# Kernel tuning notes

Measured on AMD Instinct MI355X. Metric: run time of the kernel, lower is better.

Reference implementation:

```python
import jax, jax.numpy as jnp
import numpy as np

N = 8192
E_DIM = 256
HID = 256
OUT = 128
N_PRED = 2_000_000


def setup_inputs() -> dict:
    key = jax.random.key(0)
    ks = jax.random.split(key, 6)
    node_indices = jnp.arange(N, dtype=jnp.int64) if jax.config.jax_enable_x64 else jnp.arange(N, dtype=jnp.int32)
    attn_matrix = jax.random.normal(ks[0], (N, N), dtype=jnp.float32)
    edge_label_index = jax.random.randint(ks[1], (2, N_PRED), 0, N)
    emb = jax.random.normal(ks[2], (N, E_DIM), dtype=jnp.float32) * 0.05
    W1 = jax.random.normal(ks[3], (E_DIM, HID), dtype=jnp.float32) * (1.0 / np.sqrt(E_DIM))
    b1 = jnp.zeros((HID,), dtype=jnp.float32)
    W2 = jax.random.normal(ks[4], (HID, OUT), dtype=jnp.float32) * (1.0 / np.sqrt(HID))
    b2 = jnp.zeros((OUT,), dtype=jnp.float32)
    return {"node_indices": node_indices, "attn_matrix": attn_matrix,
            "edge_label_index": edge_label_index, "emb": emb,
            "W1": W1, "b1": b1, "W2": W2, "b2": b2}


def reference(node_indices, attn_matrix, edge_label_index, emb, W1, b1, W2, b2):
    # dense_to_sparse of an (almost surely) all-nonzero dense matrix keeps all
    # N^2 edges (incl. diagonal), so no extra self-loops are added by gcn_norm.
    w = jax.nn.relu(attn_matrix)                       # edge weights after F.relu
    deg = w.sum(axis=0)                                # deg[j] = sum_i w[i,j] (scatter on col)
    dis = jnp.where(deg > 0, jax.lax.rsqrt(deg), 0.0)  # deg^{-1/2}, inf -> 0
    a_norm = dis[:, None] * w * dis[None, :]           # norm_ij = d_i^-1/2 w_ij d_j^-1/2

    x = emb[node_indices]                              # embedding lookup [N, E_DIM]
    # GCNConv: aggregate transformed features at target (col): out = A_norm^T @ (x W) + b
    h = jax.nn.relu(a_norm.T @ (x @ W1) + b1)          # [N, HID]
    z = a_norm.T @ (h @ W2) + b2                       # [N, OUT]

    # decode: dot product between endpoint embeddings
    scores = jnp.einsum('ed,ed->e', z[edge_label_index[0]], z[edge_label_index[1]])
    return scores
```

## Files before the change

### kernel.cpp

```cpp
#include <hip/hip_runtime.h>

typedef _Float16 half8  __attribute__((ext_vector_type(8)));
typedef _Float16 half4v __attribute__((ext_vector_type(4)));
typedef _Float16 half2v __attribute__((ext_vector_type(2)));
typedef float    floatx4 __attribute__((ext_vector_type(4)));
typedef float    f4v     __attribute__((ext_vector_type(4)));

#define NND 8192
#define PA  40
#define PT  136

__device__ __forceinline__ int swzk(int m, int k) { return k ^ (((m >> 3) & 3) << 3); }

#define GLOAD16(gp, lp) __builtin_amdgcn_global_load_lds(                        \
    (const __attribute__((address_space(1))) void*)(gp),                         \
    (__attribute__((address_space(3))) void*)(lp), 16, 0, 0)

#define VMCNT0() asm volatile("s_waitcnt vmcnt(0)" ::: "memory")

__global__ __launch_bounds__(256) void k_degT(const float* __restrict__ A,
                                              _Float16* __restrict__ Wh,
                                              float* __restrict__ deg) {
    __shared__ _Float16 T[128 * PT];
    __shared__ float sdeg[8 * 128];
    int t  = threadIdx.x;
    int j0 = blockIdx.x * 128, i0 = blockIdx.y * 128;
    int c = t & 31;
    int g = t >> 5;

    f4v s = {0.f, 0.f, 0.f, 0.f};
    #pragma unroll
    for (int p = 0; p < 2; ++p) {
        int rb = 64 * p + 8 * g;
        f4v v[8];
        #pragma unroll
        for (int rr = 0; rr < 8; ++rr)
            v[rr] = *(const f4v*)(A + (size_t)(i0 + rb + rr) * NND + j0 + 4 * c);
        #pragma unroll
        for (int rr = 0; rr < 8; ++rr)
            #pragma unroll
            for (int u = 0; u < 4; ++u) v[rr][u] = fmaxf(v[rr][u], 0.f);
        #pragma unroll
        for (int u = 0; u < 4; ++u) {
            half8 hv;
            #pragma unroll
            for (int rr = 0; rr < 8; ++rr) { hv[rr] = (_Float16)v[rr][u]; s[u] += v[rr][u]; }
            *(half8*)(&T[(4 * c + u) * PT + rb]) = hv;
        }
    }
    *(f4v*)(&sdeg[g * 128 + 4 * c]) = s;
    __syncthreads();

    if (t < 128) {
        float d = 0.f;
        #pragma unroll
        for (int g2 = 0; g2 < 8; ++g2) d += sdeg[g2 * 128 + t];
        atomicAdd(&deg[j0 + t], d);
    }

    #pragma unroll
    for (int p = 0; p < 8; ++p) {
        int j  = 16 * p + (t >> 4);
        int ic = (t & 15) * 8;
        half8 hv = *(const half8*)(&T[j * PT + ic]);
        *(half8*)(Wh + (size_t)(j0 + j) * NND + i0 + ic) = hv;
    }
}

__global__ __launch_bounds__(256) void k_dis(const float* __restrict__ deg, float* __restrict__ dis) {
    int j = blockIdx.x * 256 + threadIdx.x;
    float d = deg[j];
    dis[j] = d > 0.f ? 1.f / sqrtf(d) : 0.f;
}

template <typename AT>
__global__ __launch_bounds__(256) void k_mm_small(
    const AT* __restrict__ Abase, const int* __restrict__ gather,
    const float* __restrict__ B, int NB,
    _Float16* __restrict__ outT, const float* __restrict__ dis, float out_scale) {

    __shared__ _Float16 As[128 * PA];
    __shared__ _Float16 Bs[64 * PA];

    int t  = threadIdx.x;
    int i0 = blockIdx.x * 128;
    int n0 = blockIdx.y * 64;

    int am = t & 127, akh = t >> 7;
    int row = i0 + am;
    if (gather) row = gather[row];
    const AT* arow = Abase + (size_t)row * 256;

    int tp = t & 15, kp = t >> 4;

    int lane = t & 63, w = t >> 6;
    int wm = w & 1, wn = w >> 1;
    int lm = lane & 15, q = lane >> 4;

    floatx4 acc[4][2];
    #pragma unroll
    for (int a = 0; a < 4; ++a)
        #pragma unroll
        for (int b = 0; b < 2; ++b) acc[a][b] = (floatx4){0.f, 0.f, 0.f, 0.f};

    for (int ks = 0; ks < 8; ++ks) {
        int c0 = ks * 32;

        half8 av[2];
        if constexpr (sizeof(AT) == 4) {
            #pragma unroll
            for (int cc = 0; cc < 2; ++cc) {
                f4v v0 = *(const f4v*)(arow + c0 + akh * 16 + cc * 8);
                f4v v1 = *(const f4v*)(arow + c0 + akh * 16 + cc * 8 + 4);
                half8 hv;
                #pragma unroll
                for (int e = 0; e < 4; ++e) {
                    hv[e]     = (_Float16)(16.f * v0[e]);
                    hv[4 + e] = (_Float16)(16.f * v1[e]);
                }
                av[cc] = hv;
            }
        } else {
            av[0] = *(const half8*)(arow + c0 + akh * 16);
            av[1] = *(const half8*)(arow + c0 + akh * 16 + 8);
        }

        const float* bp = B + (size_t)(c0 + 2 * kp) * NB + n0 + 4 * tp;
        f4v r0 = *(const f4v*)bp;
        f4v r1 = *(const f4v*)(bp + NB);

        __syncthreads();
        #pragma unroll
        for (int cc = 0; cc < 2; ++cc) {
            int k = akh * 16 + cc * 8;
            *(half8*)(&As[am * PA + swzk(am, k)]) = av[cc];
        }
        #pragma unroll
        for (int u = 0; u < 4; ++u) {
            int n = 4 * tp + u;
            half2v p = {(_Float16)r0[u], (_Float16)r1[u]};
            *(half2v*)(&Bs[n * PA + swzk(n, 2 * kp)]) = p;
        }
        __syncthreads();

        half8 af[4], bf[2];
        #pragma unroll
        for (int mt = 0; mt < 4; ++mt) {
            int m = wm * 64 + mt * 16 + lm;
            af[mt] = *(const half8*)(&As[m * PA + swzk(m, q * 8)]);
        }
        #pragma unroll
        for (int nt = 0; nt < 2; ++nt) {
            int n = wn * 32 + nt * 16 + lm;
            bf[nt] = *(const half8*)(&Bs[n * PA + swzk(n, q * 8)]);
        }
        #pragma unroll
        for (int mt = 0; mt < 4; ++mt)
            #pragma unroll
            for (int nt = 0; nt < 2; ++nt)
                acc[mt][nt] = __builtin_amdgcn_mfma_f32_16x16x32_f16(af[mt], bf[nt], acc[mt][nt], 0, 0, 0);
    }

    #pragma unroll
    for (int mt = 0; mt < 4; ++mt) {
        int ib = i0 + wm * 64 + mt * 16 + q * 4;
        #pragma unroll
        for (int nt = 0; nt < 2; ++nt) {
            int n = n0 + wn * 32 + nt * 16 + lm;
            #pragma unroll
            for (int r = 0; r < 4; ++r) {
                float v = acc[mt][nt][r] * dis[ib + r] * out_scale;
                outT[(size_t)n * NND + ib + r] = (_Float16)v;
            }
        }
    }
}

template <int BN>
__global__ __launch_bounds__(256) void k_mm_big(
    const _Float16* __restrict__ Wh, const _Float16* __restrict__ Bt, float* __restrict__ Cp) {

    __shared__ __align__(16) _Float16 As[2 * 128 * 32];
    __shared__ __align__(16) _Float16 Bs[2 * 128 * 32];

    int t = threadIdx.x;
    int j0 = blockIdx.x * 128;
    int n0 = blockIdx.y * 128;
    size_t i_begin = (size_t)blockIdx.z * 1024;
    float* C = Cp + (size_t)blockIdx.z * (size_t)NND * BN;

    int lane = t & 63, w = t >> 6;
    int wm = w & 1, wn = w >> 1;
    int lm = lane & 15, q = lane >> 4;

    int srow = lane >> 2;
    int scol = (lane & 3) * 8;
    const _Float16* aS0 = Wh + (size_t)(j0 + w * 16 + srow) * NND + i_begin + scol;
    const _Float16* aS1 = aS0 + (size_t)64 * NND;
    const _Float16* bS0 = Bt + (size_t)(n0 + w * 16 + srow) * NND + i_begin + scol;
    const _Float16* bS1 = bS0 + (size_t)64 * NND;

    char* aLb = (char*)As + w * 1024;
    char* bLb = (char*)Bs + w * 1024;

    floatx4 acc[4][4];
    #pragma unroll
    for (int a = 0; a < 4; ++a)
        #pragma unroll
        for (int b = 0; b < 4; ++b) acc[a][b] = (floatx4){0.f, 0.f, 0.f, 0.f};

    {
        GLOAD16(aS0, aLb);
        GLOAD16(aS1, aLb + 4096);
        GLOAD16(bS0, bLb);
        GLOAD16(bS1, bLb + 4096);
    }
    VMCNT0();
    __builtin_amdgcn_s_barrier();

    for (int ks = 0; ks < 32; ++ks) {
        int cur = ks & 1;
        const _Float16* Ab = As + cur * 4096;
        const _Float16* Bb = Bs + cur * 4096;

        if (ks < 31) {
            int ko = (ks + 1) * 32;
            char* aL = aLb + (cur ^ 1) * 8192;
            char* bL = bLb + (cur ^ 1) * 8192;
            GLOAD16(aS0 + ko, aL);
            GLOAD16(aS1 + ko, aL + 4096);
            GLOAD16(bS0 + ko, bL);
            GLOAD16(bS1 + ko, bL + 4096);
        }

        half8 af[4], bf[4];
        #pragma unroll
        for (int mt = 0; mt < 4; ++mt) {
            int m = wm * 64 + mt * 16 + lm;
            af[mt] = *(const half8*)(&Ab[m * 32 + q * 8]);
        }
        #pragma unroll
        for (int nt = 0; nt < 4; ++nt) {
            int n = wn * 64 + nt * 16 + lm;
            bf[nt] = *(const half8*)(&Bb[n * 32 + q * 8]);
        }
        #pragma unroll
        for (int mt = 0; mt < 4; ++mt)
            #pragma unroll
            for (int nt = 0; nt < 4; ++nt)
                acc[mt][nt] = __builtin_amdgcn_mfma_f32_16x16x32_f16(af[mt], bf[nt], acc[mt][nt], 0, 0, 0);

        VMCNT0();
        __builtin_amdgcn_s_barrier();
    }

    #pragma unroll
    for (int mt = 0; mt < 4; ++mt) {
        int rb = j0 + wm * 64 + mt * 16 + q * 4;
        #pragma unroll
        for (int nt = 0; nt < 4; ++nt) {
            int col = n0 + wn * 64 + nt * 16 + lm;
            #pragma unroll
            for (int r = 0; r < 4; ++r)
                C[(size_t)(rb + r) * BN + col] = acc[mt][nt][r];
        }
    }
}

template <int NSH, bool RELU>
__global__ __launch_bounds__(256) void k_finalize(const float* __restrict__ Cp, const float* __restrict__ dis,
                                                  const float* __restrict__ bias, _Float16* __restrict__ out) {
    int idx4 = (blockIdx.x * 256 + threadIdx.x) * 4;
    f4v v = {0.f, 0.f, 0.f, 0.f};
    #pragma unroll
    for (int z = 0; z < 8; ++z) {
        f4v p = *(const f4v*)(Cp + (size_t)z * (NND << NSH) + idx4);
        #pragma unroll
        for (int r = 0; r < 4; ++r) v[r] += p[r];
    }
    int j  = idx4 >> NSH;
    int n0 = idx4 & ((1 << NSH) - 1);
    float dj = dis[j] * (1.f / 1024.f);
    f4v b4 = *(const f4v*)(bias + n0);
    half4v o;
    #pragma unroll
    for (int r = 0; r < 4; ++r) {
        float x = v[r] * dj + b4[r];
        if (RELU) x = fmaxf(x, 0.f);
        o[r] = (_Float16)(x * 64.f);
    }
    *(half4v*)(out + idx4) = o;
}

__global__ __launch_bounds__(256) void k_edges(const _Float16* __restrict__ zh, const int* __restrict__ ei,
                                               float* __restrict__ out, int npred) {
    int g = (blockIdx.x * 256 + threadIdx.x) >> 4;
    int l = threadIdx.x & 15;
    if (g >= npred) return;
    int a = ei[g], b = ei[npred + g];
    half8 za = *(const half8*)(zh + (size_t)a * 128 + l * 8);
    half8 zb = *(const half8*)(zh + (size_t)b * 128 + l * 8);
    float s = 0.f;
    #pragma unroll
    for (int e = 0; e < 4; ++e) {
        half2v a2 = {za[2 * e], za[2 * e + 1]};
        half2v b2 = {zb[2 * e], zb[2 * e + 1]};
        s = __builtin_amdgcn_fdot2(a2, b2, s, false);
    }
    s += __shfl_xor(s, 1);
    s += __shfl_xor(s, 2);
    s += __shfl_xor(s, 4);
    s += __shfl_xor(s, 8);
    if (l == 0) out[g] = s * (1.f / 4096.f);
}

extern "C" void kernel_launch(void* const* d_in, const int* in_sizes, int n_in,
                              void* d_out, int out_size, void* d_ws, size_t ws_size,
                              hipStream_t stream) {
    const int*   nodes = (const int*)d_in[0];
    const float* attn  = (const float*)d_in[1];
    const int*   eidx  = (const int*)d_in[2];
    const float* emb   = (const float*)d_in[3];
    const float* W1    = (const float*)d_in[4];
    const float* b1    = (const float*)d_in[5];
    const float* W2    = (const float*)d_in[6];
    const float* b2    = (const float*)d_in[7];
    float* out = (float*)d_out;
    int npred = in_sizes[2] / 2;

    char* ws = (char*)d_ws;
    float*    deg = (float*)(ws);
    float*    dis = (float*)(ws + 0x8000);
    _Float16* Wh  = (_Float16*)(ws + 0x10000);
    float*    C1p = (float*)(ws + 0x8010000);
    float*    C2p = (float*)(ws + 0xC010000);
    _Float16* M1p = (_Float16*)(ws + 0xE010000);
    _Float16* h   = (_Float16*)(ws + 0xE410000);
    _Float16* M2p = (_Float16*)(ws + 0xE810000);
    _Float16* zh  = (_Float16*)(ws + 0xEA10000);

    hipMemsetAsync(deg, 0, 8192 * sizeof(float), stream);

    k_degT<<<dim3(64, 64), 256, 0, stream>>>(attn, Wh, deg);
    k_dis<<<32, 256, 0, stream>>>(deg, dis);

    k_mm_small<float><<<dim3(64, 4), 256, 0, stream>>>(emb, nodes, W1, 256, M1p, dis, 64.f);
    k_mm_big<256><<<dim3(64, 2, 8), 256, 0, stream>>>(Wh, M1p, C1p);
    k_finalize<8, true><<<2048, 256, 0, stream>>>(C1p, dis, b1, h);
    k_mm_small<_Float16><<<dim3(64, 2), 256, 0, stream>>>(h, nullptr, W2, 128, M2p, dis, 16.f);
    k_mm_big<128><<<dim3(64, 1, 8), 256, 0, stream>>>(Wh, M2p, C2p);
    k_finalize<7, false><<<1024, 256, 0, stream>>>(C2p, dis, b2, zh);

    k_edges<<<(npred + 15) / 16, 256, 0, stream>>>(zh, eidx, out, npred);
}
```

Before: 641.1 us.

## Swizzle transpose LDS, halve split-K for first GEMM, setprio MFMA, batch edges

```diff
diff --git a/kernel.cpp b/kernel.cpp
--- a/kernel.cpp
+++ b/kernel.cpp
@@ -8,9 +8,10 @@
 
 #define NND 8192
 #define PA  40
-#define PT  136
+#define PT  128
 
 __device__ __forceinline__ int swzk(int m, int k) { return k ^ (((m >> 3) & 3) << 3); }
+__device__ __forceinline__ int swzT(int row, int chunk) { return chunk ^ ((row >> 2) & 15); }
 
 #define GLOAD16(gp, lp) __builtin_amdgcn_global_load_lds(                        \
     (const __attribute__((address_space(1))) void*)(gp),                         \
@@ -45,7 +46,9 @@
             half8 hv;
             #pragma unroll
             for (int rr = 0; rr < 8; ++rr) { hv[rr] = (_Float16)v[rr][u]; s[u] += v[rr][u]; }
-            *(half8*)(&T[(4 * c + u) * PT + rb]) = hv;
+            int row = 4 * c + u;
+            int chunk = 8 * p + g;
+            *(half8*)(&T[row * PT + swzT(row, chunk) * 8]) = hv;
         }
     }
     *(f4v*)(&sdeg[g * 128 + 4 * c]) = s;
@@ -61,9 +64,9 @@
     #pragma unroll
     for (int p = 0; p < 8; ++p) {
         int j  = 16 * p + (t >> 4);
-        int ic = (t & 15) * 8;
-        half8 hv = *(const half8*)(&T[j * PT + ic]);
-        *(half8*)(Wh + (size_t)(j0 + j) * NND + i0 + ic) = hv;
+        int mc = t & 15;
+        half8 hv = *(const half8*)(&T[j * PT + swzT(j, mc) * 8]);
+        *(half8*)(Wh + (size_t)(j0 + j) * NND + i0 + mc * 8) = hv;
     }
 }
 
@@ -176,7 +179,7 @@
     }
 }
 
-template <int BN>
+template <int BN, int ZSTEPS>
 __global__ __launch_bounds__(256) void k_mm_big(
     const _Float16* __restrict__ Wh, const _Float16* __restrict__ Bt, float* __restrict__ Cp) {
 
@@ -186,7 +189,7 @@
     int t = threadIdx.x;
     int j0 = blockIdx.x * 128;
     int n0 = blockIdx.y * 128;
-    size_t i_begin = (size_t)blockIdx.z * 1024;
+    size_t i_begin = (size_t)blockIdx.z * (ZSTEPS * 32);
     float* C = Cp + (size_t)blockIdx.z * (size_t)NND * BN;
 
     int lane = t & 63, w = t >> 6;
@@ -218,12 +221,12 @@
     VMCNT0();
     __builtin_amdgcn_s_barrier();
 
-    for (int ks = 0; ks < 32; ++ks) {
+    for (int ks = 0; ks < ZSTEPS; ++ks) {
         int cur = ks & 1;
         const _Float16* Ab = As + cur * 4096;
         const _Float16* Bb = Bs + cur * 4096;
 
-        if (ks < 31) {
+        if (ks < ZSTEPS - 1) {
             int ko = (ks + 1) * 32;
             char* aL = aLb + (cur ^ 1) * 8192;
             char* bL = bLb + (cur ^ 1) * 8192;
@@ -244,11 +247,13 @@
             int n = wn * 64 + nt * 16 + lm;
             bf[nt] = *(const half8*)(&Bb[n * 32 + q * 8]);
         }
+        __builtin_amdgcn_s_setprio(1);
         #pragma unroll
         for (int mt = 0; mt < 4; ++mt)
             #pragma unroll
             for (int nt = 0; nt < 4; ++nt)
                 acc[mt][nt] = __builtin_amdgcn_mfma_f32_16x16x32_f16(af[mt], bf[nt], acc[mt][nt], 0, 0, 0);
+        __builtin_amdgcn_s_setprio(0);
 
         VMCNT0();
         __builtin_amdgcn_s_barrier();
@@ -267,13 +272,13 @@
     }
 }
 
-template <int NSH, bool RELU>
+template <int NSH, bool RELU, int NZ>
 __global__ __launch_bounds__(256) void k_finalize(const float* __restrict__ Cp, const float* __restrict__ dis,
                                                   const float* __restrict__ bias, _Float16* __restrict__ out) {
     int idx4 = (blockIdx.x * 256 + threadIdx.x) * 4;
     f4v v = {0.f, 0.f, 0.f, 0.f};
     #pragma unroll
-    for (int z = 0; z < 8; ++z) {
+    for (int z = 0; z < NZ; ++z) {
         f4v p = *(const f4v*)(Cp + (size_t)z * (NND << NSH) + idx4);
         #pragma unroll
         for (int r = 0; r < 4; ++r) v[r] += p[r];
@@ -294,24 +299,28 @@
 
 __global__ __launch_bounds__(256) void k_edges(const _Float16* __restrict__ zh, const int* __restrict__ ei,
                                                float* __restrict__ out, int npred) {
-    int g = (blockIdx.x * 256 + threadIdx.x) >> 4;
+    int g0 = ((blockIdx.x * 256 + threadIdx.x) >> 4) * 4;
     int l = threadIdx.x & 15;
-    if (g >= npred) return;
-    int a = ei[g], b = ei[npred + g];
-    half8 za = *(const half8*)(zh + (size_t)a * 128 + l * 8);
-    half8 zb = *(const half8*)(zh + (size_t)b * 128 + l * 8);
-    float s = 0.f;
     #pragma unroll
     for (int e = 0; e < 4; ++e) {
-        half2v a2 = {za[2 * e], za[2 * e + 1]};
-        half2v b2 = {zb[2 * e], zb[2 * e + 1]};
-        s = __builtin_amdgcn_fdot2(a2, b2, s, false);
-    }
-    s += __shfl_xor(s, 1);
-    s += __shfl_xor(s, 2);
-    s += __shfl_xor(s, 4);
-    s += __shfl_xor(s, 8);
-    if (l == 0) out[g] = s * (1.f / 4096.f);
+        int g = g0 + e;
+        if (g >= npred) return;
+        int a = ei[g], b = ei[npred + g];
+        half8 za = *(const half8*)(zh + (size_t)a * 128 + l * 8);
+        half8 zb = *(const half8*)(zh + (size_t)b * 128 + l * 8);
+        float s = 0.f;
+        #pragma unroll
+        for (int u = 0; u < 4; ++u) {
+            half2v a2 = {za[2 * u], za[2 * u + 1]};
+            half2v b2 = {zb[2 * u], zb[2 * u + 1]};
+            s = __builtin_amdgcn_fdot2(a2, b2, s, false);
+        }
+        s += __shfl_xor(s, 1);
+        s += __shfl_xor(s, 2);
+        s += __shfl_xor(s, 4);
+        s += __shfl_xor(s, 8);
+        if (l == 0) out[g] = s * (1.f / 4096.f);
+    }
 }
 
 extern "C" void kernel_launch(void* const* d_in, const int* in_sizes, int n_in,
@@ -345,11 +354,11 @@
     k_dis<<<32, 256, 0, stream>>>(deg, dis);
 
     k_mm_small<float><<<dim3(64, 4), 256, 0, stream>>>(emb, nodes, W1, 256, M1p, dis, 64.f);
-    k_mm_big<256><<<dim3(64, 2, 8), 256, 0, stream>>>(Wh, M1p, C1p);
-    k_finalize<8, true><<<2048, 256, 0, stream>>>(C1p, dis, b1, h);
+    k_mm_big<256, 64><<<dim3(64, 2, 4), 256, 0, stream>>>(Wh, M1p, C1p);
+    k_finalize<8, true, 4><<<2048, 256, 0, stream>>>(C1p, dis, b1, h);
     k_mm_small<_Float16><<<dim3(64, 2), 256, 0, stream>>>(h, nullptr, W2, 128, M2p, dis, 16.f);
-    k_mm_big<128><<<dim3(64, 1, 8), 256, 0, stream>>>(Wh, M2p, C2p);
-    k_finalize<7, false><<<1024, 256, 0, stream>>>(C2p, dis, b2, zh);
-
-    k_edges<<<(npred + 15) / 16, 256, 0, stream>>>(zh, eidx, out, npred);
-}
+    k_mm_big<128, 32><<<dim3(64, 1, 8), 256, 0, stream>>>(Wh, M2p, C2p);
+    k_finalize<7, false, 8><<<1024, 256, 0, stream>>>(C2p, dis, b2, zh);
+
+    k_edges<<<(npred + 63) / 64, 256, 0, stream>>>(zh, eidx, out, npred);
+}
```

After: 605.2 us. -5.6%, faster.
